# Kernel tuning notes

Measured on AMD Instinct MI355X. Metric: run time of the kernel, lower is better.

The kernel has to match this reference:

```python
import jax, jax.numpy as jnp
import numpy as np

EPS = 1e-6

def _normalize(x):
    # x / sqrt(max(||x||^2, eps)) -- matches torch clamp_min on squared norm
    n2 = jnp.sum(x * x, axis=-1, keepdims=True)
    return x / jnp.sqrt(jnp.maximum(n2, EPS))

def setup_inputs() -> dict:
    key = jax.random.key(0)
    k1, k2, k3, k4 = jax.random.split(key, 4)
    B, N, M, D = 2, 4096, 4096, 256
    state_dim, out_dim = 2 * D, 512
    em1 = jax.random.normal(k1, (B, N, D), dtype=jnp.float32)
    em2 = jax.random.normal(k2, (B, M, D), dtype=jnp.float32)
    # fc params (torch Linear init: U(-1/sqrt(in), 1/sqrt(in)))
    bound = 1.0 / np.sqrt(state_dim)
    W = jax.random.uniform(k3, (out_dim, state_dim), minval=-bound, maxval=bound, dtype=jnp.float32)
    b = jax.random.uniform(k4, (out_dim,), minval=-bound, maxval=bound, dtype=jnp.float32)
    return {"em1": em1, "em2": em2, "W": W, "b": b}

def reference(em1, em2, W, b):
    # cosine similarity = normalized GEMM (same math as broadcast mul+sum)
    s = jnp.einsum('bnd,bmd->bnm', _normalize(em1), _normalize(em2))  # [B,N,M]
    soft = jax.nn.softmax(s, axis=-1)
    x = jnp.einsum('bnm,bmd->bnd', soft, em2)                          # [B,N,D]
    emb = jnp.concatenate([em1, x], axis=-1)                           # [B,N,2D]
    h = jax.nn.relu(emb @ W.T + b)                                     # [B,N,out_dim]
    return h
```

## Files before the change

kernel.cpp:

```cpp
#include <hip/hip_runtime.h>

#define BATCH 2
#define NQ    4096
#define MK    4096
#define DD    256
#define ODIM  512
#define SDIM  512
#define NROWS (BATCH * NQ)
#define BM    64
#define BK    64
#define MSPLIT 4
#define MCHUNK (MK / MSPLIT)
#define NKT    (MCHUNK / BK)
#define XSPLIT (BATCH * NQ * DD)

#define NCH_E1 (NROWS * DD / 8)
#define NCH_K  NCH_E1
#define NCH_V  NCH_E1
#define NCH_W  (ODIM * SDIM / 8)

typedef short bf16x8 __attribute__((ext_vector_type(8)));
typedef float f32x16 __attribute__((ext_vector_type(16)));

__device__ __forceinline__ float bf2f(unsigned short h) {
    unsigned int u = ((unsigned int)h) << 16;
    float f;
    __builtin_memcpy(&f, &u, 4);
    return f;
}
__device__ __forceinline__ unsigned short f2bf(float f) {
    unsigned int u;
    __builtin_memcpy(&u, &f, 4);
    u = (u + 0x7FFFu + ((u >> 16) & 1u)) >> 16;
    return (unsigned short)u;
}
union frag_cast { uint4 u; bf16x8 b; unsigned short h[8]; };
__device__ __forceinline__ bf16x8 ldg_frag(const unsigned short* p) {
    frag_cast c;
    c.u = *(const uint4*)p;
    return c.b;
}
__device__ __forceinline__ void load_lds16(const unsigned short* g, unsigned short* l) {
    __builtin_amdgcn_global_load_lds(
        (const __attribute__((address_space(1))) void*)g,
        (__attribute__((address_space(3))) void*)l, 16, 0, 0);
}

__global__ void rnorm_kernel(const float* em1, const float* em2, float* rn) {
    int row  = blockIdx.x * 4 + (threadIdx.x >> 6);
    int lane = threadIdx.x & 63;
    const float* src = (row < NROWS) ? em1 + (size_t)row * DD
                                     : em2 + (size_t)(row - NROWS) * DD;
    float4 v = *(const float4*)(src + lane * 4);
    float ss = v.x * v.x + v.y * v.y + v.z * v.z + v.w * v.w;
#pragma unroll
    for (int off = 1; off < 64; off <<= 1) ss += __shfl_xor(ss, off, 64);
    if (lane == 0) rn[row] = rsqrtf(fmaxf(ss, 1e-6f));
}

__global__ void swizzle_kernel(const float* em1, const float* em2, const float* W,
                               unsigned short* e1sw, unsigned short* ksw,
                               unsigned short* vsw, unsigned short* wsw) {
    int cg = blockIdx.x * 256 + threadIdx.x;
    if (cg < NCH_E1 + NCH_K) {
        const float* src;
        unsigned short* dst;
        int c0;
        if (cg < NCH_E1) { src = em1; dst = e1sw; c0 = cg; }
        else             { src = em2; dst = ksw;  c0 = cg - NCH_E1; }
        int g = c0 >> 10, c = c0 & 1023;
        int r31 = c & 31;
        int k0  = (c >> 5) * 8;
        const float* sp = src + (size_t)(g * 32 + r31) * DD + k0;
        float4 a = *(const float4*)sp;
        float4 b = *(const float4*)(sp + 4);
        ushort4 o1, o2;
        o1.x = f2bf(a.x); o1.y = f2bf(a.y); o1.z = f2bf(a.z); o1.w = f2bf(a.w);
        o2.x = f2bf(b.x); o2.y = f2bf(b.y); o2.z = f2bf(b.z); o2.w = f2bf(b.w);
        *(ushort4*)(dst + (size_t)c0 * 8)     = o1;
        *(ushort4*)(dst + (size_t)c0 * 8 + 4) = o2;
    } else if (cg < NCH_E1 + NCH_K + NCH_V) {
        int c0 = cg - (NCH_E1 + NCH_K);
        int b   = c0 >> 17;
        int r   = c0 & 131071;
        int dg  = r >> 14;
        int rr  = r & 16383;
        int oct = rr >> 5;
        int d31 = rr & 31;
        const float* sp = em2 + (size_t)(b * MK + oct * 8) * DD + dg * 32 + d31;
        ushort4 o1, o2;
        o1.x = f2bf(sp[0 * DD]); o1.y = f2bf(sp[1 * DD]);
        o1.z = f2bf(sp[2 * DD]); o1.w = f2bf(sp[3 * DD]);
        o2.x = f2bf(sp[4 * DD]); o2.y = f2bf(sp[5 * DD]);
        o2.z = f2bf(sp[6 * DD]); o2.w = f2bf(sp[7 * DD]);
        *(ushort4*)(vsw + (size_t)c0 * 8)     = o1;
        *(ushort4*)(vsw + (size_t)c0 * 8 + 4) = o2;
    } else {
        int c0 = cg - (NCH_E1 + NCH_K + NCH_V);
        if (c0 >= NCH_W) return;
        int g = c0 >> 11, c = c0 & 2047;
        int c31 = c & 31;
        int k0  = (c >> 5) * 8;
        const float* sp = W + (size_t)(g * 32 + c31) * SDIM + k0;
        float4 a = *(const float4*)sp;
        float4 b = *(const float4*)(sp + 4);
        ushort4 o1, o2;
        o1.x = f2bf(a.x); o1.y = f2bf(a.y); o1.z = f2bf(a.z); o1.w = f2bf(a.w);
        o2.x = f2bf(b.x); o2.y = f2bf(b.y); o2.z = f2bf(b.z); o2.w = f2bf(b.w);
        *(ushort4*)(wsw + (size_t)c0 * 8)     = o1;
        *(ushort4*)(wsw + (size_t)c0 * 8 + 4) = o2;
    }
}

__global__ __launch_bounds__(256, 2)
void flash_kernel(const unsigned short* e1sw, const unsigned short* ksw,
                  const unsigned short* vsw, const float* rn,
                  unsigned short* Xp, float* lbuf) {
    __shared__ unsigned short Ks[16384];
    __shared__ unsigned short Vs[16384];
    __shared__ unsigned short Ps[BM * 72];
    __shared__ float ls[2][BM];
    int tid = threadIdx.x, lane = tid & 63, w = tid >> 6;
    int l31 = lane & 31, lhalf = lane >> 5;
    int wr = w & 1, wc = w >> 1;
    int bid    = blockIdx.x;
    int mchunk = bid >> 7;
    int rowblk = bid & 127;
    int batch  = rowblk >> 6;
    int r0     = rowblk * BM;

    const unsigned short* qbase =
        e1sw + (size_t)(rowblk * 2 + wr) * 8192 + lhalf * 256 + l31 * 8;
    bf16x8 qf[16];
#pragma unroll
    for (int s = 0; s < 16; s++) qf[s] = ldg_frag(qbase + s * 512);

    float rqv[16];
#pragma unroll
    for (int i = 0; i < 16; i++) {
        int m = (i & 3) + 8 * (i >> 2) + 4 * lhalf;
        rqv[i] = rn[r0 + wr * 32 + m];
    }
    const float* rnk = rn + NROWS + batch * MK + mchunk * MCHUNK;

    const unsigned short* kchunk = ksw + (size_t)(batch * 128 + mchunk * 32) * 8192;
    const unsigned short* vbase  = vsw + (size_t)batch * 1048576 +
                                   (size_t)(mchunk * 128) * 256;

    f32x16 xacc[4];
#pragma unroll
    for (int t = 0; t < 4; t++)
#pragma unroll
        for (int i = 0; i < 16; i++) xacc[t][i] = 0.f;
    float lpart[16];
#pragma unroll
    for (int i = 0; i < 16; i++) lpart[i] = 0.f;

    for (int kt = 0; kt < NKT; kt++) {
        __syncthreads();
        {
            const unsigned short* ksrc = kchunk + (size_t)kt * 16384;
#pragma unroll
            for (int it = 0; it < 8; it++)
                load_lds16(ksrc + it * 2048 + tid * 8, &Ks[it * 2048 + tid * 8]);
            const unsigned short* vsrc = vbase + (size_t)(kt * 8) * 256;
#pragma unroll
            for (int dg = 0; dg < 8; dg++)
                load_lds16(vsrc + (size_t)dg * 131072 + tid * 8, &Vs[dg * 2048 + tid * 8]);
        }
        __syncthreads();
        f32x16 sA, sB;
#pragma unroll
        for (int i = 0; i < 16; i++) { sA[i] = 0.f; sB[i] = 0.f; }
        const unsigned short* kb = &Ks[wc * 8192 + lhalf * 256 + l31 * 8];
#pragma unroll
        for (int s = 0; s < 16; s += 2) {
            bf16x8 b0 = ldg_frag(kb + s * 512);
            bf16x8 b1 = ldg_frag(kb + (s + 1) * 512);
            sA = __builtin_amdgcn_mfma_f32_32x32x16_bf16(qf[s],     b0, sA, 0, 0, 0);
            sB = __builtin_amdgcn_mfma_f32_32x32x16_bf16(qf[s + 1], b1, sB, 0, 0, 0);
        }
        float rk = rnk[kt * BK + wc * 32 + l31];
#pragma unroll
        for (int i = 0; i < 16; i++) {
            float p = __expf((sA[i] + sB[i]) * rqv[i] * rk - 1.0f);
            unsigned short pb = f2bf(p);
            lpart[i] += bf2f(pb);
            int m = wr * 32 + (i & 3) + 8 * (i >> 2) + 4 * lhalf;
            Ps[m * 72 + wc * 32 + l31] = pb;
        }
        __syncthreads();
#pragma unroll
        for (int ks = 0; ks < 4; ks++) {
            frag_cast ac;
            ac.u = *(const uint4*)&Ps[(wr * 32 + l31) * 72 + ks * 16 + lhalf * 8];
#pragma unroll
            for (int nt = 0; nt < 4; nt++) {
                bf16x8 bf = ldg_frag(&Vs[((wc * 4 + nt) * 8 + ks * 2 + lhalf) * 256 + l31 * 8]);
                xacc[nt] = __builtin_amdgcn_mfma_f32_32x32x16_bf16(ac.b, bf, xacc[nt], 0, 0, 0);
            }
        }
    }

#pragma unroll
    for (int i = 0; i < 16; i++) {
        float v = lpart[i];
#pragma unroll
        for (int off = 1; off < 32; off <<= 1) v += __shfl_xor(v, off, 64);
        if (l31 == 0) {
            int m = wr * 32 + (i & 3) + 8 * (i >> 2) + 4 * lhalf;
            ls[wc][m] = v;
        }
    }
    __syncthreads();
    if (tid < BM)
        lbuf[(size_t)mchunk * NROWS + r0 + tid] = ls[0][tid] + ls[1][tid];

    unsigned short* xout = Xp + (size_t)mchunk * XSPLIT +
                           (size_t)(rowblk * 2 + wr) * 8192;
#pragma unroll
    for (int nt = 0; nt < 4; nt++) {
        int dcol = wc * 128 + nt * 32 + l31;
        int cbase = (dcol >> 3) * 256 + (dcol & 7);
#pragma unroll
        for (int i = 0; i < 16; i++) {
            int m = (i & 3) + 8 * (i >> 2) + 4 * lhalf;
            xout[cbase + m * 8] = f2bf(xacc[nt][i]);
        }
    }
}

__global__ void reduce_kernel(const unsigned short* Xp, const float* lbuf,
                              unsigned short* xnsw) {
    int cg  = blockIdx.x * 256 + threadIdx.x;
    int row = (cg >> 10) * 32 + (cg & 31);
    float l = lbuf[row] + lbuf[NROWS + row] +
              lbuf[2 * NROWS + row] + lbuf[3 * NROWS + row];
    float rinv = 1.0f / l;
    const unsigned short* p = Xp + (size_t)cg * 8;
    frag_cast p0, p1, p2, p3, u;
    p0.u = *(const uint4*)p;
    p1.u = *(const uint4*)(p + (size_t)XSPLIT);
    p2.u = *(const uint4*)(p + 2 * (size_t)XSPLIT);
    p3.u = *(const uint4*)(p + 3 * (size_t)XSPLIT);
#pragma unroll
    for (int j = 0; j < 8; j++) {
        float f = bf2f(p0.h[j]) + bf2f(p1.h[j]) + bf2f(p2.h[j]) + bf2f(p3.h[j]);
        u.h[j] = f2bf(f * rinv);
    }
    *(uint4*)(xnsw + (size_t)cg * 8) = u.u;
}

__global__ __launch_bounds__(256, 2)
void final_gemm(const unsigned short* e1sw, const unsigned short* xnsw,
                const unsigned short* wsw, const float* bias, float* out) {
    int tid = threadIdx.x, lane = tid & 63, w = tid >> 6;
    int l31 = lane & 31, lhalf = lane >> 5;
    int bid = blockIdx.x;
    int cb = bid & 3, rb = bid >> 2;
    int R0 = rb * 128 + 64 * (w & 1);
    int C0 = cb * 128 + 64 * (w >> 1);

    f32x16 acc[2][2];
#pragma unroll
    for (int a = 0; a < 2; a++)
#pragma unroll
        for (int b2 = 0; b2 < 2; b2++)
#pragma unroll
            for (int i = 0; i < 16; i++) acc[a][b2][i] = 0.f;

    for (int kk = 0; kk < 32; kk++) {
        bf16x8 afr[2], bfr[2];
#pragma unroll
        for (int mt = 0; mt < 2; mt++) {
            int gA = (R0 >> 5) + mt;
            const unsigned short* ap =
                (kk < 16) ? e1sw + (size_t)gA * 8192 + kk * 512
                          : xnsw + (size_t)gA * 8192 + (kk - 16) * 512;
            afr[mt] = ldg_frag(ap + lhalf * 256 + l31 * 8);
        }
#pragma unroll
        for (int nt = 0; nt < 2; nt++) {
            int gB = (C0 >> 5) + nt;
            bfr[nt] = ldg_frag(wsw + (size_t)gB * 16384 + kk * 512 + lhalf * 256 + l31 * 8);
        }
#pragma unroll
        for (int mt = 0; mt < 2; mt++)
#pragma unroll
            for (int nt = 0; nt < 2; nt++)
                acc[mt][nt] = __builtin_amdgcn_mfma_f32_32x32x16_bf16(
                    afr[mt], bfr[nt], acc[mt][nt], 0, 0, 0);
    }

#pragma unroll
    for (int nt = 0; nt < 2; nt++) {
        int col = C0 + nt * 32 + l31;
        float bb = bias[col];
#pragma unroll
        for (int mt = 0; mt < 2; mt++) {
#pragma unroll
            for (int i = 0; i < 16; i++) {
                int row = R0 + mt * 32 + (i & 3) + 8 * (i >> 2) + 4 * lhalf;
                float v = acc[mt][nt][i] + bb;
                v = v > 0.f ? v : 0.f;
                out[(size_t)row * ODIM + col] = v;
            }
        }
    }
}

extern "C" void kernel_launch(void* const* d_in, const int* in_sizes, int n_in,
                              void* d_out, int out_size, void* d_ws, size_t ws_size,
                              hipStream_t stream) {
    const float* em1  = (const float*)d_in[0];
    const float* em2  = (const float*)d_in[1];
    const float* W    = (const float*)d_in[2];
    const float* bias = (const float*)d_in[3];
    float* out = (float*)d_out;

    char* ws = (char*)d_ws;
    unsigned short* e1sw = (unsigned short*)ws;
    unsigned short* ksw  = e1sw + (size_t)NROWS * DD;
    unsigned short* vsw  = ksw  + (size_t)NROWS * DD;
    unsigned short* wsw  = vsw  + (size_t)BATCH * DD * MK;
    unsigned short* Xp   = wsw  + (size_t)ODIM * SDIM;
    unsigned short* xnsw = Xp   + 4 * (size_t)XSPLIT;
    float* lbuf = (float*)(xnsw + (size_t)NROWS * DD);
    float* rn   = lbuf + 4 * (size_t)NROWS;

    rnorm_kernel<<<(2 * NROWS) / 4, 256, 0, stream>>>(em1, em2, rn);
    swizzle_kernel<<<(NCH_E1 + NCH_K + NCH_V + NCH_W + 255) / 256, 256, 0, stream>>>(
        em1, em2, W, e1sw, ksw, vsw, wsw);
    flash_kernel<<<(NROWS / BM) * MSPLIT, 256, 0, stream>>>(e1sw, ksw, vsw, rn, Xp, lbuf);
    reduce_kernel<<<NCH_E1 / 256, 256, 0, stream>>>(Xp, lbuf, xnsw);
    final_gemm<<<(NROWS / 128) * (ODIM / 128), 256, 0, stream>>>(
        e1sw, xnsw, wsw, bias, out);
}
```

Measured before the change: 155.6 us.

## Fuse prep kernels, fold split-M reduction into final GEMM, reorder flash blocks

Merges the row-norm and swizzle kernels into one launch. Removes the separate reduce kernel: the final GEMM now sums the four split-M partial outputs and divides by the softmax denominator on the fly while loading its A operand. The final GEMM is retiled to 64x64 blocks with one 32x32 tile per wave and higher occupancy. Flash blocks are reordered so the four M-chunks of a row block run adjacently. This saves two launches and one intermediate write/read, but the partial-sum reduction is now repeated for every column block (8x) and each wave gets less operand reuse.

```diff
diff --git a/kernel.cpp b/kernel.cpp
--- a/kernel.cpp
+++ b/kernel.cpp
@@ -18,6 +18,7 @@
 #define NCH_K  NCH_E1
 #define NCH_V  NCH_E1
 #define NCH_W  (ODIM * SDIM / 8)
+#define RN_BLOCKS 4096
 
 typedef short bf16x8 __attribute__((ext_vector_type(8)));
 typedef float f32x16 __attribute__((ext_vector_type(16)));
@@ -46,22 +47,23 @@
         (__attribute__((address_space(3))) void*)l, 16, 0, 0);
 }
 
-__global__ void rnorm_kernel(const float* em1, const float* em2, float* rn) {
-    int row  = blockIdx.x * 4 + (threadIdx.x >> 6);
-    int lane = threadIdx.x & 63;
-    const float* src = (row < NROWS) ? em1 + (size_t)row * DD
-                                     : em2 + (size_t)(row - NROWS) * DD;
-    float4 v = *(const float4*)(src + lane * 4);
-    float ss = v.x * v.x + v.y * v.y + v.z * v.z + v.w * v.w;
-#pragma unroll
-    for (int off = 1; off < 64; off <<= 1) ss += __shfl_xor(ss, off, 64);
-    if (lane == 0) rn[row] = rsqrtf(fmaxf(ss, 1e-6f));
-}
-
-__global__ void swizzle_kernel(const float* em1, const float* em2, const float* W,
-                               unsigned short* e1sw, unsigned short* ksw,
-                               unsigned short* vsw, unsigned short* wsw) {
-    int cg = blockIdx.x * 256 + threadIdx.x;
+__global__ void prep_kernel(const float* em1, const float* em2, const float* W,
+                            float* rn, unsigned short* e1sw, unsigned short* ksw,
+                            unsigned short* vsw, unsigned short* wsw) {
+    int bid = blockIdx.x;
+    if (bid < RN_BLOCKS) {
+        int row  = bid * 4 + (threadIdx.x >> 6);
+        int lane = threadIdx.x & 63;
+        const float* src = (row < NROWS) ? em1 + (size_t)row * DD
+                                         : em2 + (size_t)(row - NROWS) * DD;
+        float4 v = *(const float4*)(src + lane * 4);
+        float ss = v.x * v.x + v.y * v.y + v.z * v.z + v.w * v.w;
+#pragma unroll
+        for (int off = 1; off < 64; off <<= 1) ss += __shfl_xor(ss, off, 64);
+        if (lane == 0) rn[row] = rsqrtf(fmaxf(ss, 1e-6f));
+        return;
+    }
+    int cg = (bid - RN_BLOCKS) * 256 + threadIdx.x;
     if (cg < NCH_E1 + NCH_K) {
         const float* src;
         unsigned short* dst;
@@ -124,8 +126,8 @@
     int l31 = lane & 31, lhalf = lane >> 5;
     int wr = w & 1, wc = w >> 1;
     int bid    = blockIdx.x;
-    int mchunk = bid >> 7;
-    int rowblk = bid & 127;
+    int mchunk = bid & 3;
+    int rowblk = bid >> 2;
     int batch  = rowblk >> 6;
     int r0     = rowblk * BM;
 
@@ -230,82 +232,62 @@
     }
 }
 
-__global__ void reduce_kernel(const unsigned short* Xp, const float* lbuf,
-                              unsigned short* xnsw) {
-    int cg  = blockIdx.x * 256 + threadIdx.x;
-    int row = (cg >> 10) * 32 + (cg & 31);
-    float l = lbuf[row] + lbuf[NROWS + row] +
-              lbuf[2 * NROWS + row] + lbuf[3 * NROWS + row];
-    float rinv = 1.0f / l;
-    const unsigned short* p = Xp + (size_t)cg * 8;
-    frag_cast p0, p1, p2, p3, u;
-    p0.u = *(const uint4*)p;
-    p1.u = *(const uint4*)(p + (size_t)XSPLIT);
-    p2.u = *(const uint4*)(p + 2 * (size_t)XSPLIT);
-    p3.u = *(const uint4*)(p + 3 * (size_t)XSPLIT);
-#pragma unroll
-    for (int j = 0; j < 8; j++) {
-        float f = bf2f(p0.h[j]) + bf2f(p1.h[j]) + bf2f(p2.h[j]) + bf2f(p3.h[j]);
-        u.h[j] = f2bf(f * rinv);
-    }
-    *(uint4*)(xnsw + (size_t)cg * 8) = u.u;
-}
-
-__global__ __launch_bounds__(256, 2)
-void final_gemm(const unsigned short* e1sw, const unsigned short* xnsw,
-                const unsigned short* wsw, const float* bias, float* out) {
+__global__ __launch_bounds__(256, 4)
+void final_gemm(const unsigned short* e1sw, const unsigned short* Xp,
+                const float* lbuf, const unsigned short* wsw, const float* bias,
+                float* out) {
     int tid = threadIdx.x, lane = tid & 63, w = tid >> 6;
     int l31 = lane & 31, lhalf = lane >> 5;
+    int wr = w & 1, wc = w >> 1;
     int bid = blockIdx.x;
-    int cb = bid & 3, rb = bid >> 2;
-    int R0 = rb * 128 + 64 * (w & 1);
-    int C0 = cb * 128 + 64 * (w >> 1);
-
-    f32x16 acc[2][2];
-#pragma unroll
-    for (int a = 0; a < 2; a++)
-#pragma unroll
-        for (int b2 = 0; b2 < 2; b2++)
-#pragma unroll
-            for (int i = 0; i < 16; i++) acc[a][b2][i] = 0.f;
+    int cb = bid & 7, rb = bid >> 3;
+    int gA = rb * 2 + wr;
+    int gB = cb * 2 + wc;
+
+    int rowm = gA * 32 + l31;
+    float l = lbuf[rowm] + lbuf[NROWS + rowm] +
+              lbuf[2 * NROWS + rowm] + lbuf[3 * NROWS + rowm];
+    float rinv = 1.0f / l;
+
+    f32x16 acc;
+#pragma unroll
+    for (int i = 0; i < 16; i++) acc[i] = 0.f;
+
+    const unsigned short* abase = e1sw + (size_t)gA * 8192 + lhalf * 256 + l31 * 8;
+    const unsigned short* xbase = Xp   + (size_t)gA * 8192 + lhalf * 256 + l31 * 8;
+    const unsigned short* bbase = wsw  + (size_t)gB * 16384 + lhalf * 256 + l31 * 8;
 
     for (int kk = 0; kk < 32; kk++) {
-        bf16x8 afr[2], bfr[2];
-#pragma unroll
-        for (int mt = 0; mt < 2; mt++) {
-            int gA = (R0 >> 5) + mt;
-            const unsigned short* ap =
-                (kk < 16) ? e1sw + (size_t)gA * 8192 + kk * 512
-                          : xnsw + (size_t)gA * 8192 + (kk - 16) * 512;
-            afr[mt] = ldg_frag(ap + lhalf * 256 + l31 * 8);
-        }
-#pragma unroll
-        for (int nt = 0; nt < 2; nt++) {
-            int gB = (C0 >> 5) + nt;
-            bfr[nt] = ldg_frag(wsw + (size_t)gB * 16384 + kk * 512 + lhalf * 256 + l31 * 8);
-        }
-#pragma unroll
-        for (int mt = 0; mt < 2; mt++)
-#pragma unroll
-            for (int nt = 0; nt < 2; nt++)
-                acc[mt][nt] = __builtin_amdgcn_mfma_f32_32x32x16_bf16(
-                    afr[mt], bfr[nt], acc[mt][nt], 0, 0, 0);
-    }
-
-#pragma unroll
-    for (int nt = 0; nt < 2; nt++) {
-        int col = C0 + nt * 32 + l31;
-        float bb = bias[col];
-#pragma unroll
-        for (int mt = 0; mt < 2; mt++) {
-#pragma unroll
-            for (int i = 0; i < 16; i++) {
-                int row = R0 + mt * 32 + (i & 3) + 8 * (i >> 2) + 4 * lhalf;
-                float v = acc[mt][nt][i] + bb;
-                v = v > 0.f ? v : 0.f;
-                out[(size_t)row * ODIM + col] = v;
+        bf16x8 afr;
+        if (kk < 16) {
+            afr = ldg_frag(abase + kk * 512);
+        } else {
+            const unsigned short* xp = xbase + (kk - 16) * 512;
+            frag_cast p0, p1, p2, p3, u;
+            p0.u = *(const uint4*)xp;
+            p1.u = *(const uint4*)(xp + (size_t)XSPLIT);
+            p2.u = *(const uint4*)(xp + 2 * (size_t)XSPLIT);
+            p3.u = *(const uint4*)(xp + 3 * (size_t)XSPLIT);
+#pragma unroll
+            for (int j = 0; j < 8; j++) {
+                float f = bf2f(p0.h[j]) + bf2f(p1.h[j]) +
+                          bf2f(p2.h[j]) + bf2f(p3.h[j]);
+                u.h[j] = f2bf(f * rinv);
             }
-        }
+            afr = u.b;
+        }
+        bf16x8 bfr = ldg_frag(bbase + kk * 512);
+        acc = __builtin_amdgcn_mfma_f32_32x32x16_bf16(afr, bfr, acc, 0, 0, 0);
+    }
+
+    int col = gB * 32 + l31;
+    float bb = bias[col];
+#pragma unroll
+    for (int i = 0; i < 16; i++) {
+        int row = gA * 32 + (i & 3) + 8 * (i >> 2) + 4 * lhalf;
+        float v = acc[i] + bb;
+        v = v > 0.f ? v : 0.f;
+        out[(size_t)row * ODIM + col] = v;
     }
 }
 
@@ -324,15 +306,13 @@
     unsigned short* vsw  = ksw  + (size_t)NROWS * DD;
     unsigned short* wsw  = vsw  + (size_t)BATCH * DD * MK;
     unsigned short* Xp   = wsw  + (size_t)ODIM * SDIM;
-    unsigned short* xnsw = Xp   + 4 * (size_t)XSPLIT;
-    float* lbuf = (float*)(xnsw + (size_t)NROWS * DD);
+    float* lbuf = (float*)(Xp + 4 * (size_t)XSPLIT);
     float* rn   = lbuf + 4 * (size_t)NROWS;
 
-    rnorm_kernel<<<(2 * NROWS) / 4, 256, 0, stream>>>(em1, em2, rn);
-    swizzle_kernel<<<(NCH_E1 + NCH_K + NCH_V + NCH_W + 255) / 256, 256, 0, stream>>>(
-        em1, em2, W, e1sw, ksw, vsw, wsw);
+    const int swz_blocks = (NCH_E1 + NCH_K + NCH_V + NCH_W + 255) / 256;
+    prep_kernel<<<RN_BLOCKS + swz_blocks, 256, 0, stream>>>(
+        em1, em2, W, rn, e1sw, ksw, vsw, wsw);
     flash_kernel<<<(NROWS / BM) * MSPLIT, 256, 0, stream>>>(e1sw, ksw, vsw, rn, Xp, lbuf);
-    reduce_kernel<<<NCH_E1 / 256, 256, 0, stream>>>(Xp, lbuf, xnsw);
-    final_gemm<<<(NROWS / 128) * (ODIM / 128), 256, 0, stream>>>(
-        e1sw, xnsw, wsw, bias, out);
-}
+    final_gemm<<<(NROWS / 64) * (ODIM / 64), 256, 0, stream>>>(
+        e1sw, Xp, lbuf, wsw, bias, out);
+}
```

Measured after the change: 157.5 us. Within noise of the previous version (+1.2%).
